# Kernel tuning notes

Measured on AMD Instinct MI355X. Metric: run time of the kernel, lower is better.

Reference implementation:

```python
import jax, jax.numpy as jnp
import numpy as np

B, T, I, H = 32, 512, 128, 512


def setup_inputs() -> dict:
    key = jax.random.key(0)
    ks = jax.random.split(key, 9)
    sH = 1.0 / np.sqrt(H)
    sI = 1.0 / np.sqrt(I)
    return {
        "values": jax.random.normal(ks[0], (B, T, I), jnp.float32),
        "Deltas": jax.random.uniform(ks[1], (B, T, 1), jnp.float32),
        "ys": jax.random.normal(ks[2], (B, T, 1), jnp.float32),
        # LSTMCell params (torch gate order: i, f, g, o)
        "W_ih": jax.random.uniform(ks[3], (4 * H, I), jnp.float32, -sH, sH),
        "W_hh": jax.random.uniform(ks[4], (4 * H, H), jnp.float32, -sH, sH),
        "b_ih": jax.random.uniform(ks[5], (4 * H,), jnp.float32, -sH, sH),
        "b_hh": jax.random.uniform(ks[6], (4 * H,), jnp.float32, -sH, sH),
        # atten_linear: input_size -> input_size
        "atten_W": jax.random.uniform(ks[7], (I, I), jnp.float32, -sI, sI),
        "atten_b": jax.random.uniform(ks[8], (I,), jnp.float32, -sI, sI),
    }


def lstm_cell(x, h, c, W_ih, W_hh, b_ih, b_hh):
    gates = x @ W_ih.T + b_ih + h @ W_hh.T + b_hh
    i, f, g, o = jnp.split(gates, 4, axis=-1)
    c_new = jax.nn.sigmoid(f) * c + jax.nn.sigmoid(i) * jnp.tanh(g)
    h_new = jax.nn.sigmoid(o) * jnp.tanh(c_new)
    return h_new, c_new


def reference(values, Deltas, ys, W_ih, W_hh, b_ih, b_hh, atten_W, atten_b):
    Bs, Ts, Is = values.shape
    Hs = W_hh.shape[1]
    dt = values.dtype
    # cumulative time gaps and pairwise decay matrix D[b,t,j] = cum[t] - cum[j]
    dcum = jnp.cumsum(Deltas, axis=-2)[..., 0]          # [B,T]
    D = dcum[:, :, None] - dcum[:, None, :]             # [B,T,T]
    # attention scores: linear(values) @ original_values^T
    v = values @ atten_W.T + atten_b                    # [B,T,I]
    a_tj = jnp.einsum('bti,bsi->bts', v, values)        # [B,T,T]
    # t = 0 step with zero initial state
    h0 = jnp.zeros((Bs, Hs), dt)
    c0 = jnp.zeros((Bs, Hs), dt)
    h, c = lstm_cell(v[:, 0], h0, c0, W_ih, W_hh, b_ih, b_hh)
    c_n = jnp.zeros((Bs, Ts, Hs), dt).at[:, 0].set(c)
    idx = jnp.arange(Ts)
    NEG = jnp.finfo(dt).min
    e = jnp.asarray(np.e, dt)

    def step(carry, t):
        h, c_n = carry
        mask = idx < t                                   # causal window j < t
        logits = jnp.where(mask, a_tj[:, t], NEG)
        alpha = jax.nn.softmax(logits, axis=-1)          # masked entries ~0
        w = jnp.where(mask, 1.0 / jnp.log(e + D[:, t]), 0.0)
        alpha = alpha * w
        C = jnp.einsum('bj,bjh->bh', alpha, c_n)         # weighted cell history
        h_new, c_new = lstm_cell(v[:, t], h, C, W_ih, W_hh, b_ih, b_hh)
        return (h_new, c_n.at[:, t].set(c_new)), h_new

    (_, _), hs = jax.lax.scan(step, (h, c_n), jnp.arange(1, Ts))
    h_n = jnp.concatenate([h[:, None], jnp.swapaxes(hs, 0, 1)], axis=1)
    return h_n
```

## Files before the change

### kernel.cpp

```cpp
#include <hip/hip_runtime.h>
#include <math.h>

#define B_  32
#define T_  512
#define I_  128
#define H_  512
#define G4_ 2048
#define GB_ 64

__global__ __launch_bounds__(256) void gemm_abt(
    const float* __restrict__ A, const float* __restrict__ Bm, float* __restrict__ C,
    const float* __restrict__ bias, long sA, long sB, long sC, int ldc)
{
  __shared__ float Al[64][65];
  __shared__ float Bl[64][65];
  const long z = blockIdx.z;
  A += z * sA; Bm += z * sB; C += z * sC;
  const int m0 = blockIdx.x * 64, n0 = blockIdx.y * 64;
  const int tid = threadIdx.x;
  const int tx = tid & 15, ty = tid >> 4;
  float acc[4][4] = {};

  for (int h = 0; h < 2; ++h) {
    const int k0 = h * 64;
    __syncthreads();
    #pragma unroll
    for (int s = 0; s < 4; ++s) {
      int idx = tid + s * 256;
      int m  = idx >> 4;
      int k4 = (idx & 15) << 2;
      float4 a4 = *(const float4*)&A[(long)(m0 + m) * 128 + k0 + k4];
      Al[k4 + 0][m] = a4.x; Al[k4 + 1][m] = a4.y; Al[k4 + 2][m] = a4.z; Al[k4 + 3][m] = a4.w;
      float4 b4 = *(const float4*)&Bm[(long)(n0 + m) * 128 + k0 + k4];
      Bl[k4 + 0][m] = b4.x; Bl[k4 + 1][m] = b4.y; Bl[k4 + 2][m] = b4.z; Bl[k4 + 3][m] = b4.w;
    }
    __syncthreads();
    #pragma unroll 8
    for (int k = 0; k < 64; ++k) {
      float a0 = Al[k][ty*4+0], a1 = Al[k][ty*4+1], a2 = Al[k][ty*4+2], a3 = Al[k][ty*4+3];
      float b0 = Bl[k][tx*4+0], b1 = Bl[k][tx*4+1], b2 = Bl[k][tx*4+2], b3 = Bl[k][tx*4+3];
      acc[0][0] += a0*b0; acc[0][1] += a0*b1; acc[0][2] += a0*b2; acc[0][3] += a0*b3;
      acc[1][0] += a1*b0; acc[1][1] += a1*b1; acc[1][2] += a1*b2; acc[1][3] += a1*b3;
      acc[2][0] += a2*b0; acc[2][1] += a2*b1; acc[2][2] += a2*b2; acc[2][3] += a2*b3;
      acc[3][0] += a3*b0; acc[3][1] += a3*b1; acc[3][2] += a3*b2; acc[3][3] += a3*b3;
    }
  }
  #pragma unroll
  for (int i = 0; i < 4; ++i) {
    #pragma unroll
    for (int j = 0; j < 4; ++j) {
      float bb = bias ? bias[n0 + tx*4 + j] : 0.f;
      C[(long)(m0 + ty*4 + i) * ldc + n0 + tx*4 + j] = acc[i][j] + bb;
    }
  }
}

__global__ __launch_bounds__(512) void cumsum_k(const float* __restrict__ Deltas,
                                                float* __restrict__ dcum)
{
  __shared__ float s[512];
  const int b = blockIdx.x, t = threadIdx.x;
  s[t] = Deltas[b * 512 + t];
  __syncthreads();
  for (int off = 1; off < 512; off <<= 1) {
    float v = (t >= off) ? s[t - off] : 0.f;
    __syncthreads();
    s[t] += v;
    __syncthreads();
  }
  dcum[b * 512 + t] = s[t];
}

__global__ __launch_bounds__(64) void softmax_k(float* __restrict__ a,
                                                const float* __restrict__ dcum)
{
  const int t = blockIdx.x, b = blockIdx.y;
  float* row = a + ((long)b * T_ + t) * T_;
  const int lane = threadIdx.x;
  if (t == 0) {
    #pragma unroll
    for (int i = 0; i < 8; ++i) row[i * 64 + lane] = 0.f;
    return;
  }
  float vals[8];
  float mx = -3.4e38f;
  #pragma unroll
  for (int i = 0; i < 8; ++i) {
    int j = i * 64 + lane;
    float v = (j < t) ? row[j] : -3.4e38f;
    vals[i] = v; mx = fmaxf(mx, v);
  }
  #pragma unroll
  for (int off = 1; off < 64; off <<= 1) mx = fmaxf(mx, __shfl_xor(mx, off));
  float sum = 0.f;
  #pragma unroll
  for (int i = 0; i < 8; ++i) {
    int j = i * 64 + lane;
    float e = (j < t) ? expf(vals[i] - mx) : 0.f;
    vals[i] = e; sum += e;
  }
  #pragma unroll
  for (int off = 1; off < 64; off <<= 1) sum += __shfl_xor(sum, off);
  const float E = 2.718281828459045f;
  const float dct = dcum[b * 512 + t];
  const float inv = 1.f / sum;
  #pragma unroll
  for (int i = 0; i < 8; ++i) {
    int j = i * 64 + lane;
    float w = (j < t) ? 1.f / logf(E + dct - dcum[b * 512 + j]) : 0.f;
    row[j] = vals[i] * inv * w;
  }
}

__device__ __forceinline__ void st_wt(float* p, float v) {
  __hip_atomic_store(p, v, __ATOMIC_RELAXED, __HIP_MEMORY_SCOPE_AGENT);
}
__device__ __forceinline__ float ld_wt(const float* p) {
  return __hip_atomic_load(p, __ATOMIC_RELAXED, __HIP_MEMORY_SCOPE_AGENT);
}
__device__ __forceinline__ void flag_set(unsigned* f, unsigned v) {
  __hip_atomic_store(f, v, __ATOMIC_RELAXED, __HIP_MEMORY_SCOPE_AGENT);
}
__device__ __forceinline__ int poll64(const unsigned* flags, unsigned target,
                                      unsigned* abrt) {
  long spins = 0;
  for (;;) {
    unsigned f = __hip_atomic_load(&flags[threadIdx.x], __ATOMIC_RELAXED,
                                   __HIP_MEMORY_SCOPE_AGENT);
    if (__all((int)(f >= target))) return 0;
    if (((++spins) & 63) == 0) {
      if (__hip_atomic_load(abrt, __ATOMIC_RELAXED, __HIP_MEMORY_SCOPE_AGENT)) return 1;
      if (spins > 1500000L) {
        __hip_atomic_store(abrt, 1u, __ATOMIC_RELAXED, __HIP_MEMORY_SCOPE_AGENT);
        return 1;
      }
    }
    __builtin_amdgcn_s_sleep(1);
  }
}

__global__ __launch_bounds__(256, 1) void recurrent_k(
    const float* __restrict__ v_buf,
    const float* __restrict__ alpha,
    const float* __restrict__ W_ih,
    const float* __restrict__ W_hh,
    const float* __restrict__ b_ih, const float* __restrict__ b_hh,
    float* gates,
    float* out,
    unsigned* bar)
{
  extern __shared__ float lds[];
  float* hv  = lds;
  float* cn  = lds + 8 * 512;
  float* red = cn + 512 * 64;
  __shared__ int s_ab;

  const int tid = threadIdx.x;
  const int g = blockIdx.x;
  const int grp = g >> 6;
  const int bg = grp;
  const int rs = g & 63;
  const int b_u = g >> 3, hs = g & 7;
  const int r_l = tid >> 3, cg = tid & 7;
  const int row = rs * 32 + r_l;
  const int jg = tid >> 6, l = tid & 63;

  unsigned* flagA = bar;
  unsigned* flagB = bar + 256;
  unsigned* abrt  = bar + 512;
  const unsigned* fA = flagA + grp * 64;
  const unsigned* fB = flagB + grp * 64;

  float4 wh[16];
  #pragma unroll
  for (int k = 0; k < 16; ++k)
    wh[k] = *(const float4*)&W_hh[(long)row * H_ + cg * 4 + k * 32];
  float4 wv[4];
  #pragma unroll
  for (int k = 0; k < 4; ++k)
    wv[k] = *(const float4*)&W_ih[(long)row * I_ + cg * 4 + k * 32];
  const float bias = b_ih[row] + b_hh[row];

  float vacc[8];
  #pragma unroll
  for (int bp = 0; bp < 8; ++bp) {
    float a = 0.f;
    #pragma unroll
    for (int k = 0; k < 4; ++k) {
      float4 x = *(const float4*)&v_buf[((long)(bg * 8 + bp) * T_) * I_ + cg * 4 + k * 32];
      a += wv[k].x * x.x + wv[k].y * x.y + wv[k].z * x.z + wv[k].w * x.w;
    }
    vacc[bp] = a;
  }

  for (int t = 0; t < T_; ++t) {
    if (tid < 64) { int ab = poll64(fA, (unsigned)t, abrt); if (tid == 0) s_ab = ab; }
    __syncthreads();
    if (s_ab) return;

    if (t > 0) {
      #pragma unroll
      for (int s = 0; s < 16; ++s) {
        int idx = tid + s * 256;
        int bp = idx >> 9, c = idx & 511;
        hv[bp * 512 + c] = ld_wt(&out[((long)(bg * 8 + bp) * T_ + (t - 1)) * H_ + c]);
      }
      __syncthreads();
    }

    float acc[8];
    #pragma unroll
    for (int bp = 0; bp < 8; ++bp) acc[bp] = vacc[bp];
    if (t > 0) {
      #pragma unroll
      for (int k = 0; k < 16; ++k) {
        float4 w4 = wh[k];
        #pragma unroll
        for (int bp = 0; bp < 8; ++bp) {
          float4 x = *(const float4*)&hv[bp * 512 + cg * 4 + k * 32];
          acc[bp] += w4.x * x.x + w4.y * x.y + w4.z * x.z + w4.w * x.w;
        }
      }
    }
    #pragma unroll
    for (int off = 1; off < 8; off <<= 1) {
      #pragma unroll
      for (int bp = 0; bp < 8; ++bp) acc[bp] += __shfl_xor(acc[bp], off);
    }
    if (cg == 0) {
      #pragma unroll
      for (int bp = 0; bp < 8; ++bp)
        st_wt(&gates[(long)(bg * 8 + bp) * G4_ + row], acc[bp] + bias);
    }
    __syncthreads();
    if (tid == 0) flag_set(&flagB[g], (unsigned)(t + 1));

    if (t + 1 < T_) {
      #pragma unroll
      for (int bp = 0; bp < 8; ++bp) {
        float a = 0.f;
        #pragma unroll
        for (int k = 0; k < 4; ++k) {
          float4 x = *(const float4*)&v_buf[((long)(bg * 8 + bp) * T_ + (t + 1)) * I_ + cg * 4 + k * 32];
          a += wv[k].x * x.x + wv[k].y * x.y + wv[k].z * x.z + wv[k].w * x.w;
        }
        vacc[bp] = a;
      }
    }
    float partial = 0.f;
    {
      const float* arow = alpha + ((long)b_u * T_ + t) * T_;
      int j0 = jg * 128, j1 = j0 + 128; if (j1 > t) j1 = t;
      for (int j = j0; j < j1; ++j)
        partial += arow[j] * cn[j * 64 + l];
    }
    red[tid] = partial;

    if (tid < 64) { int ab = poll64(fB, (unsigned)(t + 1), abrt); if (tid == 0) s_ab = ab; }
    __syncthreads();
    if (s_ab) return;

    if (tid < 64) {
      const long gb = (long)b_u * G4_ + hs * 64 + l;
      float gi = ld_wt(&gates[gb]);
      float gf = ld_wt(&gates[gb + H_]);
      float gg = ld_wt(&gates[gb + 2 * H_]);
      float go = ld_wt(&gates[gb + 3 * H_]);
      float C  = red[l] + red[64 + l] + red[128 + l] + red[192 + l];
      float si = 1.f / (1.f + expf(-gi));
      float sf = 1.f / (1.f + expf(-gf));
      float so = 1.f / (1.f + expf(-go));
      float cnew = sf * C + si * tanhf(gg);
      float hnew = so * tanhf(cnew);
      st_wt(&out[((long)b_u * T_ + t) * H_ + hs * 64 + l], hnew);
      cn[t * 64 + l] = cnew;
    }
    __syncthreads();
    if (tid == 0) flag_set(&flagA[g], (unsigned)(t + 1));
  }
}

extern "C" void kernel_launch(void* const* d_in, const int* in_sizes, int n_in,
                              void* d_out, int out_size, void* d_ws, size_t ws_size,
                              hipStream_t stream)
{
  const float* values  = (const float*)d_in[0];
  const float* Deltas  = (const float*)d_in[1];
  const float* W_ih    = (const float*)d_in[3];
  const float* W_hh    = (const float*)d_in[4];
  const float* b_ih    = (const float*)d_in[5];
  const float* b_hh    = (const float*)d_in[6];
  const float* atten_W = (const float*)d_in[7];
  const float* atten_b = (const float*)d_in[8];
  float* out = (float*)d_out;

  char* ws = (char*)d_ws;
  unsigned* bar = (unsigned*)ws;
  float* v_buf  = (float*)(ws + 4096);
  float* a_buf  = (float*)(ws + 4096 + 8388608);
  float* dcum   = (float*)(ws + 4096 + 8388608 + 33554432);
  float* gates  = (float*)(ws + 4096 + 8388608 + 33554432 + 65536);

  hipMemsetAsync(bar, 0, 4096, stream);

  gemm_abt<<<dim3(256, 2, 1), 256, 0, stream>>>(values, atten_W, v_buf, atten_b,
                                                0, 0, 0, 128);
  cumsum_k<<<32, 512, 0, stream>>>(Deltas, dcum);
  gemm_abt<<<dim3(8, 8, 32), 256, 0, stream>>>(v_buf, values, a_buf, nullptr,
                                               512L * 128, 512L * 128, 512L * 512, 512);
  softmax_k<<<dim3(512, 32), 64, 0, stream>>>(a_buf, dcum);

  (void)hipFuncSetAttribute((const void*)recurrent_k,
                            hipFuncAttributeMaxDynamicSharedMemorySize, 148480);
  recurrent_k<<<256, 256, 148480, stream>>>(v_buf, a_buf, W_ih, W_hh, b_ih, b_hh,
                                            gates, out, bar);
}
```

Measured before the change: 17.18 ms.

## Replace all-to-all flag polling with leader-aggregated padded mailbox barriers

Each of the 64 blocks in a group previously polled all 64 peer flags every phase. Now one leader block per phase polls the peers' flags, which are padded to 64-byte stride, and writes per-block mailbox flags that each block polls individually. This is meant to cut polling traffic and cache-line contention on shared flag lines. In exchange it adds a serial hop through the leader on the critical path of every step, and it lowers the spin timeout, which raises the risk of a spurious abort.

Measured after the change: 17.12 ms. About the same (-0.3%).

```diff
diff --git a/kernel.cpp b/kernel.cpp
--- a/kernel.cpp
+++ b/kernel.cpp
@@ -118,19 +118,21 @@
 __device__ __forceinline__ float ld_wt(const float* p) {
   return __hip_atomic_load(p, __ATOMIC_RELAXED, __HIP_MEMORY_SCOPE_AGENT);
 }
-__device__ __forceinline__ void flag_set(unsigned* f, unsigned v) {
-  __hip_atomic_store(f, v, __ATOMIC_RELAXED, __HIP_MEMORY_SCOPE_AGENT);
-}
-__device__ __forceinline__ int poll64(const unsigned* flags, unsigned target,
-                                      unsigned* abrt) {
+__device__ __forceinline__ void stflag(unsigned* p, unsigned v) {
+  __hip_atomic_store(p, v, __ATOMIC_RELAXED, __HIP_MEMORY_SCOPE_AGENT);
+}
+__device__ __forceinline__ unsigned ldflag(const unsigned* p) {
+  return __hip_atomic_load(p, __ATOMIC_RELAXED, __HIP_MEMORY_SCOPE_AGENT);
+}
+__device__ __forceinline__ int pollv(const unsigned* p, unsigned target,
+                                     unsigned* abrt) {
   long spins = 0;
   for (;;) {
-    unsigned f = __hip_atomic_load(&flags[threadIdx.x], __ATOMIC_RELAXED,
-                                   __HIP_MEMORY_SCOPE_AGENT);
+    unsigned f = ldflag(p);
     if (__all((int)(f >= target))) return 0;
     if (((++spins) & 63) == 0) {
-      if (__hip_atomic_load(abrt, __ATOMIC_RELAXED, __HIP_MEMORY_SCOPE_AGENT)) return 1;
-      if (spins > 1500000L) {
+      if (ldflag(abrt)) return 1;
+      if (spins > 400000L) {
         __hip_atomic_store(abrt, 1u, __ATOMIC_RELAXED, __HIP_MEMORY_SCOPE_AGENT);
         return 1;
       }
@@ -165,11 +167,13 @@
   const int row = rs * 32 + r_l;
   const int jg = tid >> 6, l = tid & 63;
 
-  unsigned* flagA = bar;
-  unsigned* flagB = bar + 256;
-  unsigned* abrt  = bar + 512;
-  const unsigned* fA = flagA + grp * 64;
-  const unsigned* fB = flagB + grp * 64;
+  unsigned* pflagA = bar;
+  unsigned* pflagB = bar + 4096;
+  unsigned* mailA  = bar + 8192;
+  unsigned* mailB  = bar + 12288;
+  unsigned* abrt   = bar + 16384;
+  const int LA = grp * 64, LB = grp * 64 + 1;
+  const int gl = grp * 64 + (tid & 63);
 
   float4 wh[16];
   #pragma unroll
@@ -194,7 +198,10 @@
   }
 
   for (int t = 0; t < T_; ++t) {
-    if (tid < 64) { int ab = poll64(fA, (unsigned)t, abrt); if (tid == 0) s_ab = ab; }
+    if (tid < 64) {
+      int ab = pollv(&mailA[(long)g * 16], (unsigned)t, abrt);
+      if (tid == 0) s_ab = ab;
+    }
     __syncthreads();
     if (s_ab) return;
 
@@ -233,7 +240,12 @@
         st_wt(&gates[(long)(bg * 8 + bp) * G4_ + row], acc[bp] + bias);
     }
     __syncthreads();
-    if (tid == 0) flag_set(&flagB[g], (unsigned)(t + 1));
+    if (tid == 0) stflag(&pflagB[(long)g * 16], (unsigned)(t + 1));
+
+    if (g == LB && tid < 64) {
+      int ab = pollv(&pflagB[(long)gl * 16], (unsigned)(t + 1), abrt);
+      if (!ab) stflag(&mailB[(long)gl * 16], (unsigned)(t + 1));
+    }
 
     if (t + 1 < T_) {
       #pragma unroll
@@ -256,7 +268,10 @@
     }
     red[tid] = partial;
 
-    if (tid < 64) { int ab = poll64(fB, (unsigned)(t + 1), abrt); if (tid == 0) s_ab = ab; }
+    if (tid < 64) {
+      int ab = pollv(&mailB[(long)g * 16], (unsigned)(t + 1), abrt);
+      if (tid == 0) s_ab = ab;
+    }
     __syncthreads();
     if (s_ab) return;
 
@@ -276,7 +291,12 @@
       cn[t * 64 + l] = cnew;
     }
     __syncthreads();
-    if (tid == 0) flag_set(&flagA[g], (unsigned)(t + 1));
+    if (tid == 0) stflag(&pflagA[(long)g * 16], (unsigned)(t + 1));
+
+    if (g == LA && tid < 64) {
+      int ab = pollv(&pflagA[(long)gl * 16], (unsigned)(t + 1), abrt);
+      if (!ab) stflag(&mailA[(long)gl * 16], (unsigned)(t + 1));
+    }
   }
 }
 
@@ -296,12 +316,12 @@
 
   char* ws = (char*)d_ws;
   unsigned* bar = (unsigned*)ws;
-  float* v_buf  = (float*)(ws + 4096);
-  float* a_buf  = (float*)(ws + 4096 + 8388608);
-  float* dcum   = (float*)(ws + 4096 + 8388608 + 33554432);
-  float* gates  = (float*)(ws + 4096 + 8388608 + 33554432 + 65536);
-
-  hipMemsetAsync(bar, 0, 4096, stream);
+  float* v_buf  = (float*)(ws + 69632);
+  float* a_buf  = (float*)(ws + 69632 + 8388608);
+  float* dcum   = (float*)(ws + 69632 + 8388608 + 33554432);
+  float* gates  = (float*)(ws + 69632 + 8388608 + 33554432 + 65536);
+
+  hipMemsetAsync(bar, 0, 69632, stream);
 
   gemm_abt<<<dim3(256, 2, 1), 256, 0, stream>>>(values, atten_W, v_buf, atten_b,
                                                 0, 0, 0, 128);
```
